# Kernel tuning notes

Hardware: AMD Instinct MI355X
Metric: run time of the kernel (lower is better)

Reference implementation:

```python
import jax, jax.numpy as jnp
import numpy as np

DX = 0.01
DT = 0.5
MU_UP = 0.001

_lap = np.array([[0,0,-1/12,0,0],[0,0,4/3,0,0],[-1/12,4/3,-5,4/3,-1/12],[0,0,4/3,0,0],[0,0,-1/12,0,0]], dtype=np.float32)
_dx = np.array([[0,0,1/12,0,0],[0,0,-8/12,0,0],[0,0,0,0,0],[0,0,8/12,0,0],[0,0,-1/12,0,0]], dtype=np.float32)
K_LAP = jnp.asarray(_lap)[None, None] / (DX * DX)   # [1,1,5,5]
K_DX = jnp.asarray(_dx)[None, None] / DX             # derivative along H axis (torch res_dx)
K_DY = jnp.swapaxes(K_DX, 2, 3)                      # derivative along W axis (torch res_dy)


def _conv(x, k):
    # cross-correlation, VALID, NCHW -- matches torch Conv2d
    return jax.lax.conv_general_dilated(x, k, (1, 1), 'VALID',
                                        dimension_numbers=('NCHW', 'OIHW', 'NCHW'))


def _pad(h):
    # periodic padding of 2 on both spatial dims (torch.cat based circular pad)
    return jnp.pad(h, ((0, 0), (0, 0), (2, 2), (2, 2)), mode='wrap')


def _f_rhs(u, v, Re, UA, UB, VA, VB):
    up, vp = _pad(u), _pad(v)
    u_x, u_y = _conv(up, K_DX), _conv(up, K_DY)
    v_x, v_y = _conv(vp, K_DX), _conv(vp, K_DY)
    nu = MU_UP / Re
    f_u = nu * _conv(up, K_LAP) + UA * u * u_x + UB * v * u_y
    f_v = nu * _conv(vp, K_LAP) + VA * u * v_x + VB * v * v_y
    return f_u, f_v


def setup_inputs() -> dict:
    key = jax.random.key(0)
    k_h, k_re, k_ua, k_ub, k_va, k_vb = jax.random.split(key, 6)
    h = jax.random.normal(k_h, (8, 2, 1024, 1024), dtype=jnp.float32)
    Re = jax.random.uniform(k_re, (), jnp.float32, 0.5, 1.5)  # keep 1/Re well-conditioned
    UA = jax.random.uniform(k_ua, (), jnp.float32)
    UB = jax.random.uniform(k_ub, (), jnp.float32)
    VA = jax.random.uniform(k_va, (), jnp.float32)
    VB = jax.random.uniform(k_vb, (), jnp.float32)
    return {'h': h, 'Re': Re, 'UA': UA, 'UB': UB, 'VA': VA, 'VB': VB}


def reference(h, Re, UA, UB, VA, VB):
    u0 = h[:, 0:1]
    v0 = h[:, 1:2]
    k1u, k1v = _f_rhs(u0, v0, Re, UA, UB, VA, VB)
    k2u, k2v = _f_rhs(u0 + k1u * (DT / 2.0), v0 + k1v * (DT / 2.0), Re, UA, UB, VA, VB)
    k3u, k3v = _f_rhs(u0 + k2u * (DT / 2.0), v0 + k2v * (DT / 2.0), Re, UA, UB, VA, VB)
    k4u, k4v = _f_rhs(u0 + k3u * DT, v0 + k3v * DT, Re, UA, UB, VA, VB)
    u_next = u0 + DT * (k1u + 2 * k2u + 2 * k3u + k4u) / 6.0
    v_next = v0 + DT * (k1v + 2 * k2v + 2 * k3v + k4v) / 6.0
    return jnp.concatenate((u_next, v_next), axis=1)
```

## Files before the change

### kernel.cpp

```cpp
#include <hip/hip_runtime.h>


typedef float f4 __attribute__((ext_vector_type(4)));
typedef float f2 __attribute__((ext_vector_type(2)));

#define LCOLS 88
#define LROWS 84
#define NBUF  (LROWS*LCOLS)
#define NT    320

__global__ __launch_bounds__(NT, 2)
void rk4_stencil(const float* __restrict__ h,
                 const float* __restrict__ sRe, const float* __restrict__ sUA,
                 const float* __restrict__ sUB, const float* __restrict__ sVA,
                 const float* __restrict__ sVB, float* __restrict__ out)
{
    __shared__ __align__(16) float tu[NBUF];
    __shared__ __align__(16) float tv[NBUF];

    const int tid = threadIdx.x;
    const int tc = blockIdx.x, tr = blockIdx.y, bb = blockIdx.z;

    const float Re = sRe[0], UA = sUA[0], UB = sUB[0], VA = sVA[0], VB = sVB[0];
    const float nu = 0.001f / Re;

    const float d1 = 800.f/12.f;
    const float d2 = 100.f/12.f;
    const float a1 = (4.f/3.f)*1.0e4f;
    const float a2 = -(1.f/12.f)*1.0e4f;
    const float a0 = -5.0e4f;

    const f4 z4 = {0.f, 0.f, 0.f, 0.f};

    for (int i = tid; i < NBUF/4; i += NT) { ((f4*)tu)[i] = z4; ((f4*)tv)[i] = z4; }
    __syncthreads();

    const size_t plane = 1048576;
    const float* uin = h + (size_t)(bb*2) * plane;
    const float* vin = uin + plane;
    const int base_r = tr*64 - 8, base_c = tc*64 - 8;

#pragma unroll
    for (int m = 0; m < 5; ++m) {
        int g = tid + NT*m;
        int r = g / 20, k = g - r*20;
        int gr = (base_r + r) & 1023;
        int gc = (base_c + 4*k) & 1023;
        int l = (r+2)*LCOLS + 4 + 4*k;
        *(f4*)(tu + l) = *(const f4*)(uin + (size_t)gr*1024 + gc);
        *(f4*)(tv + l) = *(const f4*)(vin + (size_t)gr*1024 + gc);
    }
    __syncthreads();

    const int c  = tid % 20;
    const int rg = tid / 20;
    const int l0 = (rg*5 + 2)*LCOLS + 4 + 4*c;

    f4 u0s[5], v0s[5], us[5], vs[5], au[5], av[5];
#pragma unroll
    for (int k = 0; k < 5; ++k) {
        u0s[k] = *(const f4*)(tu + l0 + k*LCOLS);
        v0s[k] = *(const f4*)(tv + l0 + k*LCOLS);
        us[k] = u0s[k]; vs[k] = v0s[k];
        au[k] = z4; av[k] = z4;
    }

    float* outu = out + (size_t)(bb*2) * plane;
    float* outv = outu + plane;
    const bool col_ok = (c >= 2 && c < 18);

#pragma unroll
    for (int s = 0; s < 4; ++s) {
        const float wgt  = (s == 1 || s == 2) ? 2.f : 1.f;
        const float cadd = (s <= 1) ? 0.25f : 0.5f;

        f4 t2u = *(const f4*)(tu + l0 - 2*LCOLS);
        f4 t1u = *(const f4*)(tu + l0 - 1*LCOLS);
        f4 b1u = *(const f4*)(tu + l0 + 5*LCOLS);
        f4 b2u = *(const f4*)(tu + l0 + 6*LCOLS);
        f4 t2v = *(const f4*)(tv + l0 - 2*LCOLS);
        f4 t1v = *(const f4*)(tv + l0 - 1*LCOLS);
        f4 b1v = *(const f4*)(tv + l0 + 5*LCOLS);
        f4 b2v = *(const f4*)(tv + l0 + 6*LCOLS);

        f4 nus[5], nvs[5];
#pragma unroll
        for (int k = 0; k < 5; ++k) {
            const int lk = l0 + k*LCOLS;
            f2 ulf = *(const f2*)(tu + lk - 2);
            f2 urf = *(const f2*)(tu + lk + 4);
            f2 vlf = *(const f2*)(tv + lk - 2);
            f2 vrf = *(const f2*)(tv + lk + 4);

            f4 un1 = (k >= 1) ? us[k-1] : t1u;
            f4 un2 = (k >= 2) ? us[k-2] : ((k == 1) ? t1u : t2u);
            f4 uS1 = (k <= 3) ? us[k+1] : b1u;
            f4 uS2 = (k <= 2) ? us[k+2] : ((k == 3) ? b1u : b2u);
            f4 vn1 = (k >= 1) ? vs[k-1] : t1v;
            f4 vn2 = (k >= 2) ? vs[k-2] : ((k == 1) ? t1v : t2v);
            f4 vS1 = (k <= 3) ? vs[k+1] : b1v;
            f4 vS2 = (k <= 2) ? vs[k+2] : ((k == 3) ? b1v : b2v);

            f4 uc = us[k], vc = vs[k];
            float hu[8] = {ulf[0],ulf[1],uc[0],uc[1],uc[2],uc[3],urf[0],urf[1]};
            float hv[8] = {vlf[0],vlf[1],vc[0],vc[1],vc[2],vc[3],vrf[0],vrf[1]};

            f4 fu4, fv4;
#pragma unroll
            for (int j = 0; j < 4; ++j) {
                float u = hu[j+2], v = hv[j+2];
                float urow = d1*(uS1[j]-un1[j]) + d2*(un2[j]-uS2[j]);
                float vrow = d1*(vS1[j]-vn1[j]) + d2*(vn2[j]-vS2[j]);
                float ucol = d1*(hu[j+3]-hu[j+1]) + d2*(hu[j]-hu[j+4]);
                float vcol = d1*(hv[j+3]-hv[j+1]) + d2*(hv[j]-hv[j+4]);
                float ulap = a1*((un1[j]+uS1[j])+(hu[j+1]+hu[j+3]))
                           + a2*((un2[j]+uS2[j])+(hu[j]+hu[j+4])) + a0*u;
                float vlap = a1*((vn1[j]+vS1[j])+(hv[j+1]+hv[j+3]))
                           + a2*((vn2[j]+vS2[j])+(hv[j]+hv[j+4])) + a0*v;
                fu4[j] = nu*ulap + UA*(u*urow) + UB*(v*ucol);
                fv4[j] = nu*vlap + VA*(u*vrow) + VB*(v*vcol);
            }

            if (s < 3) {
#pragma unroll
                for (int j = 0; j < 4; ++j) {
                    au[k][j] += wgt*fu4[j];
                    av[k][j] += wgt*fv4[j];
                    nus[k][j] = u0s[k][j] + cadd*fu4[j];
                    nvs[k][j] = v0s[k][j] + cadd*fv4[j];
                }
            } else {
                int r_st = rg*5 + k;
                if (col_ok && r_st >= 8 && r_st < 72) {
                    int gr = tr*64 + r_st - 8;
                    int gc = tc*64 + 4*c - 8;
                    f4 ou, ov;
#pragma unroll
                    for (int j = 0; j < 4; ++j) {
                        ou[j] = u0s[k][j] + (1.f/12.f)*(au[k][j] + fu4[j]);
                        ov[j] = v0s[k][j] + (1.f/12.f)*(av[k][j] + fv4[j]);
                    }
                    __builtin_nontemporal_store(ou, (f4*)(outu + (size_t)gr*1024 + gc));
                    __builtin_nontemporal_store(ov, (f4*)(outv + (size_t)gr*1024 + gc));
                }
            }
        }

        if (s < 3) {
            __syncthreads();
#pragma unroll
            for (int k = 0; k < 5; ++k) {
                *(f4*)(tu + l0 + k*LCOLS) = nus[k];
                *(f4*)(tv + l0 + k*LCOLS) = nvs[k];
                us[k] = nus[k]; vs[k] = nvs[k];
            }
            __syncthreads();
        }
    }
}

extern "C" void kernel_launch(void* const* d_in, const int* in_sizes, int n_in,
                              void* d_out, int out_size, void* d_ws, size_t ws_size,
                              hipStream_t stream) {
    const float* h   = (const float*)d_in[0];
    const float* sRe = (const float*)d_in[1];
    const float* sUA = (const float*)d_in[2];
    const float* sUB = (const float*)d_in[3];
    const float* sVA = (const float*)d_in[4];
    const float* sVB = (const float*)d_in[5];
    float* o = (float*)d_out;
    rk4_stencil<<<dim3(16,16,8), dim3(NT,1,1), 0, stream>>>(h, sRe, sUA, sUB, sVA, sVB, o);
}
```

Baseline: 257.8 us.

## Use 832-thread blocks with two rows per thread and recompute RK stage input from k

Raises the block to 832 threads, 800 of them active, each computing a 2-row by 4-column patch instead of 5 rows. The saved u0/v0 registers are dropped: each RK stage input is rebuilt by subtracting the previous k times its coefficient and adding the new k. The zero-fill of the shared tile is also removed. The goal is higher occupancy and fewer registers per thread. In exchange, more stencil rows are reloaded from LDS per computed row, the rebuilt stage inputs carry extra rounding, and unwritten halo cells are now left uninitialised.

```diff
diff --git a/kernel.cpp b/kernel.cpp
--- a/kernel.cpp
+++ b/kernel.cpp
@@ -7,9 +7,9 @@
 #define LCOLS 88
 #define LROWS 84
 #define NBUF  (LROWS*LCOLS)
-#define NT    320
+#define NT    832
 
-__global__ __launch_bounds__(NT, 2)
+__global__ __launch_bounds__(NT, 4)
 void rk4_stencil(const float* __restrict__ h,
                  const float* __restrict__ sRe, const float* __restrict__ sUA,
                  const float* __restrict__ sUB, const float* __restrict__ sVA,
@@ -30,129 +30,130 @@
     const float a2 = -(1.f/12.f)*1.0e4f;
     const float a0 = -5.0e4f;
 
-    const f4 z4 = {0.f, 0.f, 0.f, 0.f};
-
-    for (int i = tid; i < NBUF/4; i += NT) { ((f4*)tu)[i] = z4; ((f4*)tv)[i] = z4; }
-    __syncthreads();
-
     const size_t plane = 1048576;
     const float* uin = h + (size_t)(bb*2) * plane;
     const float* vin = uin + plane;
     const int base_r = tr*64 - 8, base_c = tc*64 - 8;
 
 #pragma unroll
-    for (int m = 0; m < 5; ++m) {
-        int g = tid + NT*m;
-        int r = g / 20, k = g - r*20;
-        int gr = (base_r + r) & 1023;
-        int gc = (base_c + 4*k) & 1023;
-        int l = (r+2)*LCOLS + 4 + 4*k;
-        *(f4*)(tu + l) = *(const f4*)(uin + (size_t)gr*1024 + gc);
-        *(f4*)(tv + l) = *(const f4*)(vin + (size_t)gr*1024 + gc);
+    for (int m = 0; m < 2; ++m) {
+        int gidx = tid + NT*m;
+        if (gidx < 1600) {
+            int r = gidx / 20, k = gidx - r*20;
+            int gr = (base_r + r) & 1023;
+            int gc = (base_c + 4*k) & 1023;
+            int l = (r+2)*LCOLS + 4 + 4*k;
+            *(f4*)(tu + l) = *(const f4*)(uin + (size_t)gr*1024 + gc);
+            *(f4*)(tv + l) = *(const f4*)(vin + (size_t)gr*1024 + gc);
+        }
     }
     __syncthreads();
 
-    const int c  = tid % 20;
-    const int rg = tid / 20;
-    const int l0 = (rg*5 + 2)*LCOLS + 4 + 4*c;
+    const bool active = tid < 800;
+    const int c = tid % 20;
+    const int g = tid / 20;
+    const int l0 = (2*g + 2)*LCOLS + 4 + 4*c;
 
-    f4 u0s[5], v0s[5], us[5], vs[5], au[5], av[5];
-#pragma unroll
-    for (int k = 0; k < 5; ++k) {
-        u0s[k] = *(const f4*)(tu + l0 + k*LCOLS);
-        v0s[k] = *(const f4*)(tv + l0 + k*LCOLS);
-        us[k] = u0s[k]; vs[k] = v0s[k];
-        au[k] = z4; av[k] = z4;
+    const f4 z4 = {0.f, 0.f, 0.f, 0.f};
+    f4 us0=z4, us1=z4, vs0=z4, vs1=z4;
+    f4 ku0=z4, ku1=z4, kv0=z4, kv1=z4;
+    f4 au0=z4, au1=z4, av0=z4, av1=z4;
+    if (active) {
+        us0 = *(const f4*)(tu + l0);
+        us1 = *(const f4*)(tu + l0 + LCOLS);
+        vs0 = *(const f4*)(tv + l0);
+        vs1 = *(const f4*)(tv + l0 + LCOLS);
     }
 
     float* outu = out + (size_t)(bb*2) * plane;
     float* outv = outu + plane;
-    const bool col_ok = (c >= 2 && c < 18);
+
+    auto stencil = [&](const f4 uc, const f4 un1, const f4 un2, const f4 uS1, const f4 uS2,
+                       const float* urow,
+                       const f4 vc, const f4 vn1, const f4 vn2, const f4 vS1, const f4 vS2,
+                       const float* vrow,
+                       f4& fu, f4& fv) {
+        f2 ulf = *(const f2*)(urow - 2);
+        f2 urf = *(const f2*)(urow + 4);
+        f2 vlf = *(const f2*)(vrow - 2);
+        f2 vrf = *(const f2*)(vrow + 4);
+        float hu[8] = {ulf[0],ulf[1],uc[0],uc[1],uc[2],uc[3],urf[0],urf[1]};
+        float hv[8] = {vlf[0],vlf[1],vc[0],vc[1],vc[2],vc[3],vrf[0],vrf[1]};
+#pragma unroll
+        for (int j = 0; j < 4; ++j) {
+            float u = hu[j+2], v = hv[j+2];
+            float udr = d1*(uS1[j]-un1[j]) + d2*(un2[j]-uS2[j]);
+            float vdr = d1*(vS1[j]-vn1[j]) + d2*(vn2[j]-vS2[j]);
+            float udc = d1*(hu[j+3]-hu[j+1]) + d2*(hu[j]-hu[j+4]);
+            float vdc = d1*(hv[j+3]-hv[j+1]) + d2*(hv[j]-hv[j+4]);
+            float ulap = a1*((un1[j]+uS1[j])+(hu[j+1]+hu[j+3]))
+                       + a2*((un2[j]+uS2[j])+(hu[j]+hu[j+4])) + a0*u;
+            float vlap = a1*((vn1[j]+vS1[j])+(hv[j+1]+hv[j+3]))
+                       + a2*((vn2[j]+vS2[j])+(hv[j]+hv[j+4])) + a0*v;
+            fu[j] = nu*ulap + UA*(u*udr) + UB*(v*udc);
+            fv[j] = nu*vlap + VA*(u*vdr) + VB*(v*vdc);
+        }
+    };
+
+    const float csub_t[4] = {0.f, 0.25f, 0.25f, 0.5f};
+    const float cadd_t[4] = {0.25f, 0.25f, 0.5f, 0.f};
+    const float wgt_t[4]  = {1.f, 2.f, 2.f, 1.f};
 
 #pragma unroll
     for (int s = 0; s < 4; ++s) {
-        const float wgt  = (s == 1 || s == 2) ? 2.f : 1.f;
-        const float cadd = (s <= 1) ? 0.25f : 0.5f;
+        if (active) {
+            const float csub = csub_t[s], cadd = cadd_t[s], wgt = wgt_t[s];
+            f4 um2 = *(const f4*)(tu + l0 - 2*LCOLS);
+            f4 um1 = *(const f4*)(tu + l0 - 1*LCOLS);
+            f4 up1 = *(const f4*)(tu + l0 + 2*LCOLS);
+            f4 up2 = *(const f4*)(tu + l0 + 3*LCOLS);
+            f4 vm2 = *(const f4*)(tv + l0 - 2*LCOLS);
+            f4 vm1 = *(const f4*)(tv + l0 - 1*LCOLS);
+            f4 vp1 = *(const f4*)(tv + l0 + 2*LCOLS);
+            f4 vp2 = *(const f4*)(tv + l0 + 3*LCOLS);
 
-        f4 t2u = *(const f4*)(tu + l0 - 2*LCOLS);
-        f4 t1u = *(const f4*)(tu + l0 - 1*LCOLS);
-        f4 b1u = *(const f4*)(tu + l0 + 5*LCOLS);
-        f4 b2u = *(const f4*)(tu + l0 + 6*LCOLS);
-        f4 t2v = *(const f4*)(tv + l0 - 2*LCOLS);
-        f4 t1v = *(const f4*)(tv + l0 - 1*LCOLS);
-        f4 b1v = *(const f4*)(tv + l0 + 5*LCOLS);
-        f4 b2v = *(const f4*)(tv + l0 + 6*LCOLS);
-
-        f4 nus[5], nvs[5];
-#pragma unroll
-        for (int k = 0; k < 5; ++k) {
-            const int lk = l0 + k*LCOLS;
-            f2 ulf = *(const f2*)(tu + lk - 2);
-            f2 urf = *(const f2*)(tu + lk + 4);
-            f2 vlf = *(const f2*)(tv + lk - 2);
-            f2 vrf = *(const f2*)(tv + lk + 4);
-
-            f4 un1 = (k >= 1) ? us[k-1] : t1u;
-            f4 un2 = (k >= 2) ? us[k-2] : ((k == 1) ? t1u : t2u);
-            f4 uS1 = (k <= 3) ? us[k+1] : b1u;
-            f4 uS2 = (k <= 2) ? us[k+2] : ((k == 3) ? b1u : b2u);
-            f4 vn1 = (k >= 1) ? vs[k-1] : t1v;
-            f4 vn2 = (k >= 2) ? vs[k-2] : ((k == 1) ? t1v : t2v);
-            f4 vS1 = (k <= 3) ? vs[k+1] : b1v;
-            f4 vS2 = (k <= 2) ? vs[k+2] : ((k == 3) ? b1v : b2v);
-
-            f4 uc = us[k], vc = vs[k];
-            float hu[8] = {ulf[0],ulf[1],uc[0],uc[1],uc[2],uc[3],urf[0],urf[1]};
-            float hv[8] = {vlf[0],vlf[1],vc[0],vc[1],vc[2],vc[3],vrf[0],vrf[1]};
-
-            f4 fu4, fv4;
-#pragma unroll
-            for (int j = 0; j < 4; ++j) {
-                float u = hu[j+2], v = hv[j+2];
-                float urow = d1*(uS1[j]-un1[j]) + d2*(un2[j]-uS2[j]);
-                float vrow = d1*(vS1[j]-vn1[j]) + d2*(vn2[j]-vS2[j]);
-                float ucol = d1*(hu[j+3]-hu[j+1]) + d2*(hu[j]-hu[j+4]);
-                float vcol = d1*(hv[j+3]-hv[j+1]) + d2*(hv[j]-hv[j+4]);
-                float ulap = a1*((un1[j]+uS1[j])+(hu[j+1]+hu[j+3]))
-                           + a2*((un2[j]+uS2[j])+(hu[j]+hu[j+4])) + a0*u;
-                float vlap = a1*((vn1[j]+vS1[j])+(hv[j+1]+hv[j+3]))
-                           + a2*((vn2[j]+vS2[j])+(hv[j]+hv[j+4])) + a0*v;
-                fu4[j] = nu*ulap + UA*(u*urow) + UB*(v*ucol);
-                fv4[j] = nu*vlap + VA*(u*vrow) + VB*(v*vcol);
-            }
+            f4 fu0, fv0, fu1, fv1;
+            stencil(us0, um1, um2, us1, up1, tu + l0,
+                    vs0, vm1, vm2, vs1, vp1, tv + l0, fu0, fv0);
+            stencil(us1, us0, um1, up1, up2, tu + l0 + LCOLS,
+                    vs1, vs0, vm1, vp1, vp2, tv + l0 + LCOLS, fu1, fv1);
 
             if (s < 3) {
 #pragma unroll
                 for (int j = 0; j < 4; ++j) {
-                    au[k][j] += wgt*fu4[j];
-                    av[k][j] += wgt*fv4[j];
-                    nus[k][j] = u0s[k][j] + cadd*fu4[j];
-                    nvs[k][j] = v0s[k][j] + cadd*fv4[j];
+                    au0[j] += wgt*fu0[j];  av0[j] += wgt*fv0[j];
+                    au1[j] += wgt*fu1[j];  av1[j] += wgt*fv1[j];
+                    us0[j] = (us0[j] - csub*ku0[j]) + cadd*fu0[j];
+                    vs0[j] = (vs0[j] - csub*kv0[j]) + cadd*fv0[j];
+                    us1[j] = (us1[j] - csub*ku1[j]) + cadd*fu1[j];
+                    vs1[j] = (vs1[j] - csub*kv1[j]) + cadd*fv1[j];
                 }
-            } else {
-                int r_st = rg*5 + k;
-                if (col_ok && r_st >= 8 && r_st < 72) {
-                    int gr = tr*64 + r_st - 8;
-                    int gc = tc*64 + 4*c - 8;
-                    f4 ou, ov;
+                ku0 = fu0; kv0 = fv0; ku1 = fu1; kv1 = fv1;
+            } else if (g >= 4 && g < 36 && c >= 2 && c < 18) {
+                int gr = tr*64 + 2*g - 8;
+                int gc = tc*64 + 4*c - 8;
+                f4 o;
 #pragma unroll
-                    for (int j = 0; j < 4; ++j) {
-                        ou[j] = u0s[k][j] + (1.f/12.f)*(au[k][j] + fu4[j]);
-                        ov[j] = v0s[k][j] + (1.f/12.f)*(av[k][j] + fv4[j]);
-                    }
-                    __builtin_nontemporal_store(ou, (f4*)(outu + (size_t)gr*1024 + gc));
-                    __builtin_nontemporal_store(ov, (f4*)(outv + (size_t)gr*1024 + gc));
-                }
+                for (int j = 0; j < 4; ++j) o[j] = (us0[j] - 0.5f*ku0[j]) + (1.f/12.f)*(au0[j] + fu0[j]);
+                __builtin_nontemporal_store(o, (f4*)(outu + (size_t)gr*1024 + gc));
+#pragma unroll
+                for (int j = 0; j < 4; ++j) o[j] = (vs0[j] - 0.5f*kv0[j]) + (1.f/12.f)*(av0[j] + fv0[j]);
+                __builtin_nontemporal_store(o, (f4*)(outv + (size_t)gr*1024 + gc));
+#pragma unroll
+                for (int j = 0; j < 4; ++j) o[j] = (us1[j] - 0.5f*ku1[j]) + (1.f/12.f)*(au1[j] + fu1[j]);
+                __builtin_nontemporal_store(o, (f4*)(outu + (size_t)(gr+1)*1024 + gc));
+#pragma unroll
+                for (int j = 0; j < 4; ++j) o[j] = (vs1[j] - 0.5f*kv1[j]) + (1.f/12.f)*(av1[j] + fv1[j]);
+                __builtin_nontemporal_store(o, (f4*)(outv + (size_t)(gr+1)*1024 + gc));
             }
         }
-
         if (s < 3) {
             __syncthreads();
-#pragma unroll
-            for (int k = 0; k < 5; ++k) {
-                *(f4*)(tu + l0 + k*LCOLS) = nus[k];
-                *(f4*)(tv + l0 + k*LCOLS) = nvs[k];
-                us[k] = nus[k]; vs[k] = nvs[k];
+            if (active) {
+                *(f4*)(tu + l0)         = us0;
+                *(f4*)(tu + l0 + LCOLS) = us1;
+                *(f4*)(tv + l0)         = vs0;
+                *(f4*)(tv + l0 + LCOLS) = vs1;
             }
             __syncthreads();
         }
```

Result: faster. 235.6 us (-8.6%).
